# Kernel tuning notes

Hardware: AMD Instinct MI355X
Metric: run time of the kernel (lower is better)

Reference implementation:

```python
import jax, jax.numpy as jnp
import numpy as np

CLASS_NUM = 4            # number of positive classes
NUM_CLASSES = CLASS_NUM + 1  # last column is the negative class
W_P = 4.0
EPS = 1e-9
THR = 0.5


def setup_inputs() -> dict:
    key = jax.random.key(0)
    k1, k2 = jax.random.split(key)
    N = 4_000_000
    x = jax.random.normal(k1, (N, NUM_CLASSES), dtype=jnp.float32)
    t = jax.random.randint(k2, (N,), 0, NUM_CLASSES)
    return {"x": x, "t": t}


def _conf_mpu_loss(x, t):
    N = x.shape[0]
    p = jax.nn.softmax(x, axis=1)                       # [N, C]
    log_pneg = jnp.log(p[:, -1] + EPS)                  # [N]

    ones = jnp.ones((N,), dtype=jnp.float32)
    counts = jax.ops.segment_sum(ones, t, num_segments=NUM_CLASSES)  # per-class counts
    prior = counts[:CLASS_NUM] / N                      # empirical priors (positive classes)

    # loss_per_class: sum over samples with t==c of -log(p[n,c]+eps)
    logp_t = jnp.log(jnp.take_along_axis(p, t[:, None], axis=1)[:, 0] + EPS)
    class_losses = jax.ops.segment_sum(-logp_t, t, num_segments=NUM_CLASSES)

    # loss_per_class_neg: sum over samples with t==i (i positive) of -log(p_neg+eps)
    loss_neg = jax.ops.segment_sum(-log_pneg, t, num_segments=NUM_CLASSES)[:CLASS_NUM]

    # conf_loss_per_class
    conf = []
    for i in range(CLASS_NUM):
        mask = (p[:, i] > THR) & (t == i)
        nsel = jnp.sum(mask.astype(jnp.float32))
        li = jnp.sum(jnp.where(mask, -log_pneg / p[:, i], 0.0))
        conf.append(li / jnp.maximum(nsel, 1.0))        # li==0 when nsel==0
    mask_n = jnp.all(p <= THR, axis=1) & (t == CLASS_NUM)
    li_n = jnp.sum(jnp.where(mask_n, -log_pneg, 0.0))
    conf_neg = li_n / jnp.maximum(counts[CLASS_NUM], 1.0)  # li_n==0 when no selection
    conf_pos = jnp.stack(conf)                          # [CLASS_NUM]

    denom = jnp.maximum(1.0, counts[:CLASS_NUM])
    risk1 = jnp.sum(prior * class_losses[:CLASS_NUM] / denom)
    risk2 = jnp.sum(prior * conf_pos)
    risk3 = jnp.sum(prior * loss_neg / denom)
    risk4 = conf_neg

    positive_risk = W_P * (risk1 + risk2 - risk3)
    positive_risk = jnp.where(positive_risk < 0, 0.0, positive_risk)
    return positive_risk + risk4


def reference(x, t):
    return _conf_mpu_loss(x, t)
```

## Files before the change

### kernel.cpp

```cpp
#include <hip/hip_runtime.h>

namespace {
constexpr int BLOCK = 256;
constexpr int GRID = 1024;
constexpr int PSTRIDE = 1024;
constexpr float WPF = 4.0f;
constexpr float LN2 = 0.69314718055994531f;
constexpr float LOG2E = 1.44269504088896340f;
}

struct Quad { float4 v0, v1, v2, v3, v4; int4 tt; };

__device__ __forceinline__ float wave_reduce(float v) {
#pragma unroll
    for (int o = 32; o > 0; o >>= 1) v += __shfl_down(v, o, 64);
    return v;
}

__global__ __launch_bounds__(BLOCK) void mpu_main(const float* __restrict__ x,
                                                  const int* __restrict__ t,
                                                  float* __restrict__ part, int N) {
    __shared__ float red[BLOCK / 64][16];

    float S13 = 0.f, li0 = 0.f, li1 = 0.f, li2 = 0.f, li3 = 0.f, liN = 0.f;
    int c0 = 0, c1 = 0, c2 = 0, c3 = 0, n0 = 0, n1 = 0, n2 = 0, n3 = 0;

    auto process = [&](float x0, float x1, float x2, float x3, float x4, int tc) {
        const float y0 = x0 * LOG2E, y1 = x1 * LOG2E, y2 = x2 * LOG2E,
                    y3 = x3 * LOG2E, y4 = x4 * LOG2E;
        const float f0 = __builtin_amdgcn_exp2f(y0);
        const float f1 = __builtin_amdgcn_exp2f(y1);
        const float f2 = __builtin_amdgcn_exp2f(y2);
        const float f3 = __builtin_amdgcn_exp2f(y3);
        const float f4 = __builtin_amdgcn_exp2f(y4);
        const float s = ((f0 + f1) + (f2 + f3)) + f4;
        const float L2 = __builtin_amdgcn_logf(s);
        const float thr = L2 - 1.0f;
        const float ymax = fmaxf(fmaxf(fmaxf(y0, y1), fmaxf(y2, y3)), y4);
        const float yt = (tc == 0) ? y0 : (tc == 1) ? y1 : (tc == 2) ? y2
                       : (tc == 3) ? y3 : y4;
        const float nltY = L2 - yt;
        const float nlnY = L2 - y4;
        const bool sel = (yt > thr);
        const bool alle = (ymax <= thr);
        const bool tpos = (tc < 4);
        S13 += tpos ? (y4 - yt) : 0.f;
        const float cv = sel ? nlnY * __builtin_amdgcn_exp2f(nltY) : 0.f;
        li0 += (tc == 0) ? cv : 0.f;
        li1 += (tc == 1) ? cv : 0.f;
        li2 += (tc == 2) ? cv : 0.f;
        li3 += (tc == 3) ? cv : 0.f;
        liN += (tc == 4 && alle) ? nlnY : 0.f;

        const unsigned long long b0 = __ballot(tc == 0);
        const unsigned long long b1 = __ballot(tc == 1);
        const unsigned long long b2 = __ballot(tc == 2);
        const unsigned long long b3 = __ballot(tc == 3);
        const unsigned long long bs = __ballot(sel);
        c0 += (int)__popcll(b0);
        c1 += (int)__popcll(b1);
        c2 += (int)__popcll(b2);
        c3 += (int)__popcll(b3);
        n0 += (int)__popcll(bs & b0);
        n1 += (int)__popcll(bs & b1);
        n2 += (int)__popcll(bs & b2);
        n3 += (int)__popcll(bs & b3);
    };

    auto load_quad = [&](int g, Quad& q) {
        const float4* xv = reinterpret_cast<const float4*>(x) + (size_t)g * 5;
        q.v0 = xv[0]; q.v1 = xv[1]; q.v2 = xv[2]; q.v3 = xv[3]; q.v4 = xv[4];
        q.tt = reinterpret_cast<const int4*>(t)[g];
    };

    auto process4 = [&](const Quad& q) {
        process(q.v0.x, q.v0.y, q.v0.z, q.v0.w, q.v1.x, q.tt.x);
        process(q.v1.y, q.v1.z, q.v1.w, q.v2.x, q.v2.y, q.tt.y);
        process(q.v2.z, q.v2.w, q.v3.x, q.v3.y, q.v3.z, q.tt.z);
        process(q.v3.w, q.v4.x, q.v4.y, q.v4.z, q.v4.w, q.tt.w);
    };

    const int pid = blockIdx.x * BLOCK + threadIdx.x;
    const int S = gridDim.x * BLOCK;
    const int nQuad = N >> 2;
    const int niter = (nQuad + S - 1) / S;

    Quad A, B;
    if (pid < nQuad) load_quad(pid, A);
    for (int it = 0; it < niter; it += 2) {
        const int g1 = pid + (it + 1) * S;
        if (g1 < nQuad) load_quad(g1, B);
        __builtin_amdgcn_sched_barrier(0);
        const int gA = pid + it * S;
        if (gA < nQuad) process4(A);
        const int g2 = pid + (it + 2) * S;
        if (g2 < nQuad) load_quad(g2, A);
        __builtin_amdgcn_sched_barrier(0);
        if (g1 < nQuad) process4(B);
    }

    if (blockIdx.x == 0 && threadIdx.x == 0) {
        for (int k = (N >> 2) << 2; k < N; ++k)
            process(x[k * 5 + 0], x[k * 5 + 1], x[k * 5 + 2], x[k * 5 + 3],
                    x[k * 5 + 4], t[k]);
    }

    const int wv = threadIdx.x >> 6, ln = threadIdx.x & 63;
    float fr[6] = {S13, li0, li1, li2, li3, liN};
#pragma unroll
    for (int j = 0; j < 6; ++j) {
        const float v = wave_reduce(fr[j]);
        if (ln == 0) red[wv][j] = v;
    }
    if (ln == 0) {
        red[wv][6] = (float)c0;   red[wv][7] = (float)c1;
        red[wv][8] = (float)c2;   red[wv][9] = (float)c3;
        red[wv][10] = (float)n0;  red[wv][11] = (float)n1;
        red[wv][12] = (float)n2;  red[wv][13] = (float)n3;
    }
    __syncthreads();
    if (threadIdx.x < 14) {
        const float v = red[0][threadIdx.x] + red[1][threadIdx.x] +
                        red[2][threadIdx.x] + red[3][threadIdx.x];
        part[threadIdx.x * PSTRIDE + blockIdx.x] = v;
    }
}

__global__ __launch_bounds__(896) void mpu_final(const float* __restrict__ part,
                                                 float* __restrict__ out,
                                                 int nb, int N) {
    __shared__ float red[16];
    const int w = threadIdx.x >> 6, ln = threadIdx.x & 63;
    float s = 0.f;
    for (int b = ln; b < nb; b += 64) s += part[w * PSTRIDE + b];
    s = wave_reduce(s);
    if (ln == 0) red[w] = s;
    __syncthreads();
    if (threadIdx.x == 0) {
        const float invN = 1.0f / (float)N;
        const float risk13 = LN2 * red[0] * invN;
        float risk2 = 0.0f;
#pragma unroll
        for (int c = 0; c < 4; ++c)
            risk2 += (red[6 + c] * invN) *
                     (LN2 * red[1 + c] / fmaxf(red[10 + c], 1.0f));
        const float c4 = (float)N - (red[6] + red[7] + red[8] + red[9]);
        const float risk4 = LN2 * red[5] / fmaxf(c4, 1.0f);
        float pos = WPF * (risk13 + risk2);
        if (pos < 0.0f) pos = 0.0f;
        out[0] = pos + risk4;
    }
}

extern "C" void kernel_launch(void* const* d_in, const int* in_sizes, int n_in,
                              void* d_out, int out_size, void* d_ws, size_t ws_size,
                              hipStream_t stream) {
    const float* x = (const float*)d_in[0];
    const int* t = (const int*)d_in[1];
    float* out = (float*)d_out;
    float* part = (float*)d_ws;
    const int N = in_sizes[1];

    const int nQuad = N >> 2;
    int grid = (nQuad + BLOCK - 1) / BLOCK;
    if (grid > GRID) grid = GRID;
    if (grid < 1) grid = 1;
    mpu_main<<<grid, BLOCK, 0, stream>>>(x, t, part, N);
    mpu_final<<<1, 896, 0, stream>>>(part, out, grid, N);
}
```

Measured before the change: 134.4 us.

## Stage x loads through shared memory for fully coalesced float4 reads

```diff
diff --git a/kernel.cpp b/kernel.cpp
--- a/kernel.cpp
+++ b/kernel.cpp
@@ -9,8 +9,6 @@
 constexpr float LOG2E = 1.44269504088896340f;
 }
 
-struct Quad { float4 v0, v1, v2, v3, v4; int4 tt; };
-
 __device__ __forceinline__ float wave_reduce(float v) {
 #pragma unroll
     for (int o = 32; o > 0; o >>= 1) v += __shfl_down(v, o, 64);
@@ -20,6 +18,7 @@
 __global__ __launch_bounds__(BLOCK) void mpu_main(const float* __restrict__ x,
                                                   const int* __restrict__ t,
                                                   float* __restrict__ part, int N) {
+    __shared__ float4 tile[BLOCK * 5];
     __shared__ float red[BLOCK / 64][16];
 
     float S13 = 0.f, li0 = 0.f, li1 = 0.f, li2 = 0.f, li3 = 0.f, liN = 0.f;
@@ -67,36 +66,52 @@
         n3 += (int)__popcll(bs & b3);
     };
 
-    auto load_quad = [&](int g, Quad& q) {
-        const float4* xv = reinterpret_cast<const float4*>(x) + (size_t)g * 5;
-        q.v0 = xv[0]; q.v1 = xv[1]; q.v2 = xv[2]; q.v3 = xv[3]; q.v4 = xv[4];
-        q.tt = reinterpret_cast<const int4*>(t)[g];
+    const int tid = threadIdx.x;
+    const int S = gridDim.x * BLOCK;
+    const int nQuad = N >> 2;
+    const int nF4 = nQuad * 5;
+    const int niter = (nQuad + S - 1) / S;
+    const float4* __restrict__ xv4 = reinterpret_cast<const float4*>(x);
+    const int4* __restrict__ tv4 = reinterpret_cast<const int4*>(t);
+
+    float4 R0, R1, R2, R3, R4;
+    int4 Rt;
+    auto issue = [&](int it) {
+        const int tstart = blockIdx.x * BLOCK + it * S;
+        const int fb = tstart * 5 + tid;
+        if (fb < nF4)        R0 = xv4[fb];
+        if (fb + 256 < nF4)  R1 = xv4[fb + 256];
+        if (fb + 512 < nF4)  R2 = xv4[fb + 512];
+        if (fb + 768 < nF4)  R3 = xv4[fb + 768];
+        if (fb + 1024 < nF4) R4 = xv4[fb + 1024];
+        if (tstart + tid < nQuad) Rt = tv4[tstart + tid];
     };
 
-    auto process4 = [&](const Quad& q) {
-        process(q.v0.x, q.v0.y, q.v0.z, q.v0.w, q.v1.x, q.tt.x);
-        process(q.v1.y, q.v1.z, q.v1.w, q.v2.x, q.v2.y, q.tt.y);
-        process(q.v2.z, q.v2.w, q.v3.x, q.v3.y, q.v3.z, q.tt.z);
-        process(q.v3.w, q.v4.x, q.v4.y, q.v4.z, q.v4.w, q.tt.w);
-    };
-
-    const int pid = blockIdx.x * BLOCK + threadIdx.x;
-    const int S = gridDim.x * BLOCK;
-    const int nQuad = N >> 2;
-    const int niter = (nQuad + S - 1) / S;
-
-    Quad A, B;
-    if (pid < nQuad) load_quad(pid, A);
-    for (int it = 0; it < niter; it += 2) {
-        const int g1 = pid + (it + 1) * S;
-        if (g1 < nQuad) load_quad(g1, B);
+    issue(0);
+    for (int it = 0; it < niter; ++it) {
+        __syncthreads();
+        tile[tid] = R0;
+        tile[tid + 256] = R1;
+        tile[tid + 512] = R2;
+        tile[tid + 768] = R3;
+        tile[tid + 1024] = R4;
+        const int4 myT = Rt;
+        const int tstart = blockIdx.x * BLOCK + it * S;
+        const bool valid = (tstart + tid) < nQuad;
+        if (it + 1 < niter) issue(it + 1);
         __builtin_amdgcn_sched_barrier(0);
-        const int gA = pid + it * S;
-        if (gA < nQuad) process4(A);
-        const int g2 = pid + (it + 2) * S;
-        if (g2 < nQuad) load_quad(g2, A);
-        __builtin_amdgcn_sched_barrier(0);
-        if (g1 < nQuad) process4(B);
+        __syncthreads();
+        if (valid) {
+            const float4 v0 = tile[tid * 5 + 0];
+            const float4 v1 = tile[tid * 5 + 1];
+            const float4 v2 = tile[tid * 5 + 2];
+            const float4 v3 = tile[tid * 5 + 3];
+            const float4 v4 = tile[tid * 5 + 4];
+            process(v0.x, v0.y, v0.z, v0.w, v1.x, myT.x);
+            process(v1.y, v1.z, v1.w, v2.x, v2.y, myT.y);
+            process(v2.z, v2.w, v3.x, v3.y, v3.z, myT.z);
+            process(v3.w, v4.x, v4.y, v4.z, v4.w, myT.w);
+        }
     }
 
     if (blockIdx.x == 0 && threadIdx.x == 0) {
```

Result: no change. 135.3 us (+0.6%).
